# Performance work log

Hardware: AMD Instinct MI355X
Metric: run time of the kernel (lower is better)

Reference implementation:

```python
import jax, jax.numpy as jnp
import numpy as np

E, C, M, H, O = 8, 4096, 1024, 4096, 1024

def setup_inputs() -> dict:
    key = jax.random.key(0)
    k = jax.random.split(key, 5)
    # kaiming-uniform-ish scales (exact init distribution not needed for correctness baseline)
    s1 = 1.0 / np.sqrt(M)
    s2 = 1.0 / np.sqrt(H)
    return {
        'x': jax.random.normal(k[0], (E, C, M), dtype=jnp.float32),
        'fc1_w': jax.random.uniform(k[1], (E, H, M), minval=-s1, maxval=s1, dtype=jnp.float32),
        'fc1_b': jax.random.uniform(k[2], (E, H), minval=-s1, maxval=s1, dtype=jnp.float32),
        'fc2_w': jax.random.uniform(k[3], (E, H, O), minval=-s2, maxval=s2, dtype=jnp.float32),
        'fc2_b': jax.random.uniform(k[4], (E, O), minval=-s2, maxval=s2, dtype=jnp.float32),
    }

def reference(x, fc1_w, fc1_b, fc2_w, fc2_b):
    # y = relu(x @ fc1_w^T + b1) @ fc2_w + b2, batched over experts e
    h = jnp.einsum('ecm,ehm->ech', x, fc1_w) + fc1_b[:, None, :]
    h = jax.nn.relu(h)
    y = jnp.einsum('ech,eho->eco', h, fc2_w) + fc2_b[:, None, :]
    return y
```

## Files before the change

kernel.cpp:

```cpp
#include <hip/hip_runtime.h>


typedef __bf16 bf16x8 __attribute__((ext_vector_type(8)));
typedef float f32x4 __attribute__((ext_vector_type(4)));

__device__ __forceinline__ unsigned short f2bf(float f) {
  union { float f; unsigned int u; } v; v.f = f;
  unsigned int u = v.u;
  u += 0x7fffu + ((u >> 16) & 1u);
  return (unsigned short)(u >> 16);
}

#define GLD_LDS16(gptr, lptr)                                               \
  __builtin_amdgcn_global_load_lds(                                         \
      (const __attribute__((address_space(1))) void*)(gptr),                \
      (__attribute__((address_space(3))) void*)(lptr), 16, 0, 0)

__global__ void cvt_bf16_kernel(const float* __restrict__ in,
                                unsigned short* __restrict__ out, long n) {
  long i = ((long)blockIdx.x * blockDim.x + threadIdx.x) * 4;
  if (i >= n) return;
  const float4 v = *(const float4*)(in + i);
  ushort4 o;
  o.x = f2bf(v.x); o.y = f2bf(v.y); o.z = f2bf(v.z); o.w = f2bf(v.w);
  *(ushort4*)(out + i) = o;
}

__global__ void transpose_cvt_kernel(const float* __restrict__ in,
                                     unsigned short* __restrict__ out,
                                     int H, int O, long istride, long ostride) {
  __shared__ unsigned short tile[32][33];
  const float* inp = in + (long)blockIdx.z * istride;
  unsigned short* outp = out + (long)blockIdx.z * ostride;
  const int o0 = blockIdx.x * 32, h0 = blockIdx.y * 32;
  const int tx = threadIdx.x, ty = threadIdx.y;
#pragma unroll
  for (int r = ty; r < 32; r += 8)
    tile[r][tx] = f2bf(inp[(long)(h0 + r) * O + o0 + tx]);
  __syncthreads();
#pragma unroll
  for (int r = ty; r < 32; r += 8)
    outp[(long)(o0 + r) * H + h0 + tx] = tile[tx][r];
}

#define BM 256
#define BN 256
#define BK 64

template <int EPI>
__global__ __launch_bounds__(512, 2) void gemm_bt_kernel(
    const unsigned short* __restrict__ A, const unsigned short* __restrict__ B,
    const float* __restrict__ bias, void* __restrict__ Cout,
    int Nd, int Kd, long sA, long sB, long sBias, long sC) {
  __shared__ unsigned short As[2][BM * BK];
  __shared__ unsigned short Bs[2][BN * BK];

  const int nbx = gridDim.x;
  const int nbxy = nbx * gridDim.y;
  const int nwg = nbxy * gridDim.z;
  int gid = blockIdx.x + nbx * blockIdx.y + nbxy * blockIdx.z;
  gid = (gid & 7) * (nwg >> 3) + (gid >> 3);
  const int bz = gid / nbxy;
  const int rem = gid - bz * nbxy;
  const int by = rem / nbx;
  const int bx = rem - by * nbx;

  const unsigned short* Ae = A + (long)bz * sA;
  const unsigned short* Be = B + (long)bz * sB;
  const float* be = bias + (long)bz * sBias;

  const int tid = threadIdx.x;
  const int wave = tid >> 6;
  const int lane = tid & 63;
  const int wm = wave >> 2;
  const int wn = wave & 3;
  const int fr = lane & 15;
  const int quad = lane >> 4;
  const int fsw = fr & 7;

  const int blockM = by * BM;
  const int blockN = bx * BN;

  const int srow = tid >> 3;
  const int skc = ((tid & 7) ^ (srow & 7)) * 8;
  const unsigned short* gA = Ae + (long)(blockM + srow) * Kd + skc;
  const unsigned short* gB = Be + (long)(blockN + srow) * Kd + skc;

#define STAGE_A(buf, band, kt)                                              \
  GLD_LDS16(gA + (long)(band) * Kd + (kt) * BK,                             \
            &As[buf][(band) * BK + wave * 512])
#define STAGE_B(buf, band, kt)                                              \
  GLD_LDS16(gB + (long)(band) * Kd + (kt) * BK,                             \
            &Bs[buf][(band) * BK + wave * 512])
#define STAGE_A_MH0(buf, kt) { STAGE_A(buf, 0, kt);   STAGE_A(buf, 128, kt); }
#define STAGE_A_MH1(buf, kt) { STAGE_A(buf, 64, kt);  STAGE_A(buf, 192, kt); }
#define STAGE_B_R0(buf, kt)  { STAGE_B(buf, 0, kt);   STAGE_B(buf, 64, kt);  }
#define STAGE_B_R1(buf, kt)  { STAGE_B(buf, 128, kt); STAGE_B(buf, 192, kt); }

#define BAR __builtin_amdgcn_s_barrier()
#define LGKM0 asm volatile("s_waitcnt lgkmcnt(0)" ::: "memory")
#define VMCNT6 asm volatile("s_waitcnt vmcnt(6)" ::: "memory")

  f32x4 acc[8][4];
#pragma unroll
  for (int a = 0; a < 8; ++a)
#pragma unroll
    for (int b = 0; b < 4; ++b) acc[a][b] = (f32x4){0.f, 0.f, 0.f, 0.f};

  const int NT = Kd / BK;

  const int aBase = (wm * 128 + fr) * BK;
  const int bBase = (wn * 64 + fr) * BK;
  const int s0 = (quad ^ fsw) * 8;
  const int s1 = ((4 + quad) ^ fsw) * 8;

  bf16x8 af[4], bw[8];

#define READ_A(bf, s)                                                       \
  {                                                                         \
    const unsigned short* _p = &As[bf][aBase + (2 * (s)) * 16 * BK];        \
    af[0] = *(const bf16x8*)(_p + s0);                                      \
    af[1] = *(const bf16x8*)(_p + s1);                                      \
    af[2] = *(const bf16x8*)(_p + 16 * BK + s0);                            \
    af[3] = *(const bf16x8*)(_p + 16 * BK + s1);                            \
  }

#define READ_B(bf)                                                          \
  {                                                                         \
    _Pragma("unroll")                                                       \
    for (int ni = 0; ni < 4; ++ni) {                                        \
      bw[2 * ni]     = *(const bf16x8*)&Bs[bf][bBase + ni * 16 * BK + s0];  \
      bw[2 * ni + 1] = *(const bf16x8*)&Bs[bf][bBase + ni * 16 * BK + s1];  \
    }                                                                       \
  }

#define MFMA_STRIPE(s)                                                      \
  __builtin_amdgcn_s_setprio(1);                                            \
  _Pragma("unroll")                                                         \
  for (int mi = 0; mi < 2; ++mi)                                            \
    _Pragma("unroll")                                                       \
    for (int ni = 0; ni < 4; ++ni) {                                        \
      acc[2 * (s) + mi][ni] = __builtin_amdgcn_mfma_f32_16x16x32_bf16(      \
          af[2 * mi], bw[2 * ni], acc[2 * (s) + mi][ni], 0, 0, 0);          \
      acc[2 * (s) + mi][ni] = __builtin_amdgcn_mfma_f32_16x16x32_bf16(      \
          af[2 * mi + 1], bw[2 * ni + 1], acc[2 * (s) + mi][ni], 0, 0, 0);  \
    }                                                                       \
  __builtin_amdgcn_s_setprio(0);

  STAGE_B_R0(0, 0);
  STAGE_B_R1(0, 0);
  STAGE_A_MH0(0, 0);
  STAGE_A_MH1(0, 0);
  STAGE_B_R0(1, 1);
  STAGE_B_R1(1, 1);
  STAGE_A_MH0(1, 1);
  VMCNT6;
  BAR;

  for (int it = 0; it < NT / 2; ++it) {
    const int U = 2 * it;
    const int kW = (U + 2 < NT) ? U + 2 : NT - 1;
    const int kX = (U + 3 < NT) ? U + 3 : NT - 1;

    READ_B(0);
    READ_A(0, 0);
    STAGE_A_MH1(1, U + 1);
    BAR; LGKM0;
    MFMA_STRIPE(0);
    BAR;

    READ_A(0, 1);
    STAGE_B_R0(0, kW);
    BAR; LGKM0;
    MFMA_STRIPE(1);
    BAR;

    READ_A(0, 2);
    STAGE_B_R1(0, kW);
    BAR; LGKM0;
    MFMA_STRIPE(2);
    BAR;

    READ_A(0, 3);
    STAGE_A_MH0(0, kW);
    BAR; LGKM0;
    MFMA_STRIPE(3);
    VMCNT6;
    BAR;

    READ_B(1);
    READ_A(1, 0);
    STAGE_A_MH1(0, kW);
    BAR; LGKM0;
    MFMA_STRIPE(0);
    BAR;

    READ_A(1, 1);
    STAGE_B_R0(1, kX);
    BAR; LGKM0;
    MFMA_STRIPE(1);
    BAR;

    READ_A(1, 2);
    STAGE_B_R1(1, kX);
    BAR; LGKM0;
    MFMA_STRIPE(2);
    BAR;

    READ_A(1, 3);
    STAGE_A_MH0(1, kX);
    BAR; LGKM0;
    MFMA_STRIPE(3);
    VMCNT6;
    BAR;
  }

  float bv[4];
#pragma unroll
  for (int ni = 0; ni < 4; ++ni) bv[ni] = be[blockN + wn * 64 + ni * 16 + fr];

  if (EPI == 0) {
    unsigned short* Co = (unsigned short*)Cout + (long)bz * sC;
#pragma unroll
    for (int mi = 0; mi < 8; ++mi) {
      const int m = blockM + wm * 128 + mi * 16 + quad * 4;
#pragma unroll
      for (int r = 0; r < 4; ++r) {
        const long rowoff = (long)(m + r) * Nd;
#pragma unroll
        for (int ni = 0; ni < 4; ++ni) {
          float v = acc[mi][ni][r] + bv[ni];
          v = v > 0.f ? v : 0.f;
          Co[rowoff + blockN + wn * 64 + ni * 16 + fr] = f2bf(v);
        }
      }
    }
  } else {
    float* Co = (float*)Cout + (long)bz * sC;
#pragma unroll
    for (int mi = 0; mi < 8; ++mi) {
      const int m = blockM + wm * 128 + mi * 16 + quad * 4;
#pragma unroll
      for (int r = 0; r < 4; ++r) {
        const long rowoff = (long)(m + r) * Nd;
#pragma unroll
        for (int ni = 0; ni < 4; ++ni)
          Co[rowoff + blockN + wn * 64 + ni * 16 + fr] = acc[mi][ni][r] + bv[ni];
      }
    }
  }
}

extern "C" void kernel_launch(void* const* d_in, const int* in_sizes, int n_in,
                              void* d_out, int out_size, void* d_ws,
                              size_t ws_size, hipStream_t stream) {
  const float* x  = (const float*)d_in[0];
  const float* w1 = (const float*)d_in[1];
  const float* b1 = (const float*)d_in[2];
  const float* w2 = (const float*)d_in[3];
  const float* b2 = (const float*)d_in[4];
  float* out = (float*)d_out;

  const int E = 8, C = 4096, M = 1024, H = 4096, O = 1024;
  const long nx  = (long)C * M;
  const long nw1 = (long)H * M;
  const long nw2 = (long)O * H;
  const long nh  = (long)C * H;

  unsigned short* ws = (unsigned short*)d_ws;
  const size_t needBatch = (size_t)(E * (nx + nw1 + nw2 + nh)) * 2;

  if (ws_size >= needBatch) {
    unsigned short* xb  = ws;
    unsigned short* w1b = xb + E * nx;
    unsigned short* w2t = w1b + E * nw1;
    unsigned short* hb  = w2t + E * nw2;
    const long tx = E * nx, tw1 = E * nw1;
    cvt_bf16_kernel<<<tx / 1024, 256, 0, stream>>>(x, xb, tx);
    cvt_bf16_kernel<<<tw1 / 1024, 256, 0, stream>>>(w1, w1b, tw1);
    transpose_cvt_kernel<<<dim3(O / 32, H / 32, E), dim3(32, 8), 0, stream>>>(
        w2, w2t, H, O, (long)H * O, (long)O * H);
    gemm_bt_kernel<0><<<dim3(H / BN, C / BM, E), 512, 0, stream>>>(
        xb, w1b, b1, hb, H, M, nx, nw1, H, nh);
    gemm_bt_kernel<1><<<dim3(O / BN, C / BM, E), 512, 0, stream>>>(
        hb, w2t, b2, out, O, H, nh, nw2, O, (long)C * O);
  } else {
    unsigned short* xb  = ws;
    unsigned short* w1b = xb + nx;
    unsigned short* w2t = w1b + nw1;
    unsigned short* hb  = w2t + nw2;
    for (int e = 0; e < E; ++e) {
      cvt_bf16_kernel<<<nx / 1024, 256, 0, stream>>>(x + e * nx, xb, nx);
      cvt_bf16_kernel<<<nw1 / 1024, 256, 0, stream>>>(w1 + e * nw1, w1b, nw1);
      transpose_cvt_kernel<<<dim3(O / 32, H / 32, 1), dim3(32, 8), 0, stream>>>(
          w2 + e * nw2, w2t, H, O, 0, 0);
      gemm_bt_kernel<0><<<dim3(H / BN, C / BM, 1), 512, 0, stream>>>(
          xb, w1b, b1 + (long)e * H, hb, H, M, 0, 0, 0, 0);
      gemm_bt_kernel<1><<<dim3(O / BN, C / BM, 1), 512, 0, stream>>>(
          hb, w2t, b2 + (long)e * O, out + e * nx, O, H, 0, 0, 0, 0);
    }
  }
}
```

Baseline: 974.7 us.

## Restructure GEMM main loop into two half-tile MFMA phases with fewer barriers

Replaces the four-stripe-per-buffer schedule with two half phases. Each phase loads four A fragments and covers both k-halves at once, and all four B bands are staged in one group, with the vmcnt wait adjusted to 8. This halves the number of barriers per iteration, removes the explicit lgkmcnt waits, and gives each phase a longer run of MFMAs between syncs. The cost is more fragment registers live at once and coarser overlap of LDS staging with compute, which may hurt occupancy or latency hiding.

```diff
diff --git a/kernel.cpp b/kernel.cpp
--- a/kernel.cpp
+++ b/kernel.cpp
@@ -94,12 +94,11 @@
             &Bs[buf][(band) * BK + wave * 512])
 #define STAGE_A_MH0(buf, kt) { STAGE_A(buf, 0, kt);   STAGE_A(buf, 128, kt); }
 #define STAGE_A_MH1(buf, kt) { STAGE_A(buf, 64, kt);  STAGE_A(buf, 192, kt); }
-#define STAGE_B_R0(buf, kt)  { STAGE_B(buf, 0, kt);   STAGE_B(buf, 64, kt);  }
-#define STAGE_B_R1(buf, kt)  { STAGE_B(buf, 128, kt); STAGE_B(buf, 192, kt); }
+#define STAGE_B_ALL(buf, kt) { STAGE_B(buf, 0, kt);   STAGE_B(buf, 64, kt);  \
+                               STAGE_B(buf, 128, kt); STAGE_B(buf, 192, kt); }
 
 #define BAR __builtin_amdgcn_s_barrier()
-#define LGKM0 asm volatile("s_waitcnt lgkmcnt(0)" ::: "memory")
-#define VMCNT6 asm volatile("s_waitcnt vmcnt(6)" ::: "memory")
+#define VMCNT8 asm volatile("s_waitcnt vmcnt(8)" ::: "memory")
 
   f32x4 acc[8][4];
 #pragma unroll
@@ -114,47 +113,47 @@
   const int s0 = (quad ^ fsw) * 8;
   const int s1 = ((4 + quad) ^ fsw) * 8;
 
-  bf16x8 af[4], bw[8];
-
-#define READ_A(bf, s)                                                       \
+  bf16x8 af[4][2], bw[4][2];
+
+#define READ_AH(bf, h)                                                      \
   {                                                                         \
-    const unsigned short* _p = &As[bf][aBase + (2 * (s)) * 16 * BK];        \
-    af[0] = *(const bf16x8*)(_p + s0);                                      \
-    af[1] = *(const bf16x8*)(_p + s1);                                      \
-    af[2] = *(const bf16x8*)(_p + 16 * BK + s0);                            \
-    af[3] = *(const bf16x8*)(_p + 16 * BK + s1);                            \
+    _Pragma("unroll")                                                       \
+    for (int mi = 0; mi < 4; ++mi) {                                        \
+      const unsigned short* _p =                                            \
+          &As[bf][aBase + ((h) * 64 + mi * 16) * BK];                       \
+      af[mi][0] = *(const bf16x8*)(_p + s0);                                \
+      af[mi][1] = *(const bf16x8*)(_p + s1);                                \
+    }                                                                       \
   }
 
 #define READ_B(bf)                                                          \
   {                                                                         \
     _Pragma("unroll")                                                       \
     for (int ni = 0; ni < 4; ++ni) {                                        \
-      bw[2 * ni]     = *(const bf16x8*)&Bs[bf][bBase + ni * 16 * BK + s0];  \
-      bw[2 * ni + 1] = *(const bf16x8*)&Bs[bf][bBase + ni * 16 * BK + s1];  \
+      const unsigned short* _p = &Bs[bf][bBase + ni * 16 * BK];             \
+      bw[ni][0] = *(const bf16x8*)(_p + s0);                                \
+      bw[ni][1] = *(const bf16x8*)(_p + s1);                                \
     }                                                                       \
   }
 
-#define MFMA_STRIPE(s)                                                      \
+#define MFMA_HALF(h)                                                        \
   __builtin_amdgcn_s_setprio(1);                                            \
   _Pragma("unroll")                                                         \
-  for (int mi = 0; mi < 2; ++mi)                                            \
+  for (int kk = 0; kk < 2; ++kk)                                            \
     _Pragma("unroll")                                                       \
-    for (int ni = 0; ni < 4; ++ni) {                                        \
-      acc[2 * (s) + mi][ni] = __builtin_amdgcn_mfma_f32_16x16x32_bf16(      \
-          af[2 * mi], bw[2 * ni], acc[2 * (s) + mi][ni], 0, 0, 0);          \
-      acc[2 * (s) + mi][ni] = __builtin_amdgcn_mfma_f32_16x16x32_bf16(      \
-          af[2 * mi + 1], bw[2 * ni + 1], acc[2 * (s) + mi][ni], 0, 0, 0);  \
-    }                                                                       \
+    for (int mi = 0; mi < 4; ++mi)                                          \
+      _Pragma("unroll")                                                     \
+      for (int ni = 0; ni < 4; ++ni)                                        \
+        acc[(h) * 4 + mi][ni] = __builtin_amdgcn_mfma_f32_16x16x32_bf16(    \
+            af[mi][kk], bw[ni][kk], acc[(h) * 4 + mi][ni], 0, 0, 0);        \
   __builtin_amdgcn_s_setprio(0);
 
-  STAGE_B_R0(0, 0);
-  STAGE_B_R1(0, 0);
+  STAGE_B_ALL(0, 0);
   STAGE_A_MH0(0, 0);
   STAGE_A_MH1(0, 0);
-  STAGE_B_R0(1, 1);
-  STAGE_B_R1(1, 1);
+  STAGE_B_ALL(1, 1);
   STAGE_A_MH0(1, 1);
-  VMCNT6;
+  VMCNT8;
   BAR;
 
   for (int it = 0; it < NT / 2; ++it) {
@@ -163,55 +162,31 @@
     const int kX = (U + 3 < NT) ? U + 3 : NT - 1;
 
     READ_B(0);
-    READ_A(0, 0);
+    READ_AH(0, 0);
     STAGE_A_MH1(1, U + 1);
-    BAR; LGKM0;
-    MFMA_STRIPE(0);
-    BAR;
-
-    READ_A(0, 1);
-    STAGE_B_R0(0, kW);
-    BAR; LGKM0;
-    MFMA_STRIPE(1);
-    BAR;
-
-    READ_A(0, 2);
-    STAGE_B_R1(0, kW);
-    BAR; LGKM0;
-    MFMA_STRIPE(2);
-    BAR;
-
-    READ_A(0, 3);
+    MFMA_HALF(0);
+    VMCNT8;
+    BAR;
+
+    READ_AH(0, 1);
+    STAGE_B_ALL(0, kW);
     STAGE_A_MH0(0, kW);
-    BAR; LGKM0;
-    MFMA_STRIPE(3);
-    VMCNT6;
+    MFMA_HALF(1);
+    VMCNT8;
     BAR;
 
     READ_B(1);
-    READ_A(1, 0);
+    READ_AH(1, 0);
     STAGE_A_MH1(0, kW);
-    BAR; LGKM0;
-    MFMA_STRIPE(0);
-    BAR;
-
-    READ_A(1, 1);
-    STAGE_B_R0(1, kX);
-    BAR; LGKM0;
-    MFMA_STRIPE(1);
-    BAR;
-
-    READ_A(1, 2);
-    STAGE_B_R1(1, kX);
-    BAR; LGKM0;
-    MFMA_STRIPE(2);
-    BAR;
-
-    READ_A(1, 3);
+    MFMA_HALF(0);
+    VMCNT8;
+    BAR;
+
+    READ_AH(1, 1);
+    STAGE_B_ALL(1, kX);
     STAGE_A_MH0(1, kX);
-    BAR; LGKM0;
-    MFMA_STRIPE(3);
-    VMCNT6;
+    MFMA_HALF(1);
+    VMCNT8;
     BAR;
   }
 
```

Measured after the change: 898.7 us. 1.08x faster.
